# Performance work log

Measured on AMD Instinct MI355X. Metric: run time of the kernel, lower is better.

## Reference

```python
import jax, jax.numpy as jnp
import numpy as np

DIM = 768; NH = 8; G = 14; N = G * G + 1; B = 64; PD = DIM // 16; HID = 4 * DIM
SCOPES = (1, 4, 7)


def _build_adj(fs, scope):
    # windowed adjacency on an fs x fs grid, padded with an always-on ACM (class) token
    idx = np.arange(fs)
    ii, jj = np.meshgrid(idx, idx, indexing='ij')
    ri, rj = ii.ravel(), jj.ravel()
    a = ((np.abs(ri[:, None] - ri[None, :]) <= scope) & (np.abs(rj[:, None] - rj[None, :]) <= scope)).astype(np.float32)
    out = np.ones((fs * fs + 1, fs * fs + 1), np.float32)
    out[1:, 1:] = a
    return out


def _prior_adj():
    # loop=0 -> loop1=loop2=0, repeat = NH//4; heads get [adj1,adj1,adj2,adj2,adj3,adj3,ones,ones]
    rep = NH // 4
    mats = [_build_adj(G, s) for s in SCOPES] + [np.ones((N, N), np.float32)]
    return np.stack([m for m in mats for _ in range(rep)], 0)


def _rel_idx():
    coords = np.stack(np.meshgrid(np.arange(G), np.arange(G), indexing='ij')).reshape(2, -1)
    rel = (coords[:, :, None] - coords[:, None, :]).transpose(1, 2, 0).copy()
    rel[..., 0] += G - 1
    rel[..., 1] += G - 1
    rel[..., 0] *= 2 * G - 1
    idx = rel.sum(-1)
    out = np.full((N, N), (2 * G - 1) ** 2 + 1, np.int32)
    out[1:, 1:] = idx
    return out


def _biases():
    r = np.arange(-G, G + 1)  # arange(1-(G+1), G+1)
    g = np.stack(np.meshgrid(r, r, indexing='ij')).reshape(2, -1).T
    return g.astype(np.float32)  # ((2G+1)^2, 2)


def setup_inputs():
    key = jax.random.key(0)
    ks = iter(jax.random.split(key, 32))
    rn = lambda *s: jax.random.normal(next(ks), s, jnp.float32) * 0.02
    return dict(
        x=jax.random.normal(next(ks), (B, N, DIM), jnp.float32),
        norm1_w=jnp.ones(DIM), norm1_b=jnp.zeros(DIM),
        qkv_w=rn(3 * DIM, DIM),
        scale=10.0 * jnp.ones((NH, 1, 1)),
        pp_w=rn(PD, 2), pp_b=jnp.zeros(PD),
        ln1_w=jnp.ones(PD), ln1_b=jnp.zeros(PD), fcp1_w=rn(PD, PD), fcp1_b=jnp.zeros(PD),
        ln2_w=jnp.ones(PD), ln2_b=jnp.zeros(PD), fcp2_w=rn(PD, PD), fcp2_b=jnp.zeros(PD),
        ln3_w=jnp.ones(PD), ln3_b=jnp.zeros(PD), fcp3_w=rn(NH, PD), fcp3_b=jnp.zeros(NH),
        pre_w=rn(NH, NH) + jnp.eye(NH), post_w=rn(NH, NH) + jnp.eye(NH),
        proj_w=rn(DIM, DIM), proj_b=jnp.zeros(DIM),
        norm2_w=jnp.ones(DIM), norm2_b=jnp.zeros(DIM),
        m1_w=rn(HID, DIM), m1_b=jnp.zeros(HID),
        m2_w=rn(DIM, HID), m2_b=jnp.zeros(DIM),
        prior_adj=jnp.asarray(_prior_adj()),
        biases=jnp.asarray(_biases()),
        rel_idx=jnp.asarray(_rel_idx()),
    )


def _ln(x, w, b, eps=1e-5):
    m = x.mean(-1, keepdims=True)
    v = ((x - m) ** 2).mean(-1, keepdims=True)
    return (x - m) / jnp.sqrt(v + eps) * w + b


def _l2n(x, eps=1e-12):
    return x / jnp.maximum(jnp.linalg.norm(x, axis=-1, keepdims=True), eps)


def reference(x, norm1_w, norm1_b, qkv_w, scale, pp_w, pp_b, ln1_w, ln1_b, fcp1_w, fcp1_b, ln2_w, ln2_b, fcp2_w, fcp2_b, ln3_w, ln3_b, fcp3_w, fcp3_b, pre_w, post_w, proj_w, proj_b, norm2_w, norm2_b, m1_w, m1_b, m2_w, m2_b, prior_adj, biases, rel_idx):
    Bq, Nq, C = x.shape
    d = C // NH
    h = _ln(x, norm1_w, norm1_b)
    qkv = (h @ qkv_w.T).reshape(Bq, Nq, 3, NH, d).transpose(2, 0, 3, 1, 4)
    q, k, v = qkv[0], qkv[1], qkv[2]  # each (B, NH, N, d)
    attn = jnp.einsum('bhnd,bhmd->bhnm', _l2n(q), _l2n(k)) * jnp.minimum(scale, 100.0)[None]
    p = biases @ pp_w.T + pp_b
    p = jax.nn.relu(_ln(p, ln1_w, ln1_b)) @ fcp1_w.T + fcp1_b
    p = jax.nn.relu(_ln(p, ln2_w, ln2_b)) @ fcp2_w.T + fcp2_b
    p = jax.nn.relu(_ln(p, ln3_w, ln3_b)) @ fcp3_w.T + fcp3_b  # (841, NH)
    rpb = p[rel_idx]  # (N, N, NH)
    attn = attn + rpb.transpose(2, 0, 1)[None]
    attn = jnp.einsum('oh,bhnm->bonm', pre_w, attn)  # 1x1 conv over heads (pre-softmax)
    attn = jnp.where(prior_adj[None] > 0, attn, -1e9)
    attn = jax.nn.softmax(attn, axis=-1)
    attn = jnp.einsum('oh,bhnm->bonm', post_w, attn)  # 1x1 conv over heads (post-softmax)
    out = jnp.einsum('bhnm,bhmd->bhnd', attn, v).transpose(0, 2, 1, 3).reshape(Bq, Nq, C)
    x = x + (out @ proj_w.T + proj_b)
    h2 = _ln(x, norm2_w, norm2_b)
    h2 = jax.nn.gelu(h2 @ m1_w.T + m1_b, approximate=False) @ m2_w.T + m2_b
    return x + h2
```

## Files before the change

kernel.cpp:

```cpp
#include <hip/hip_runtime.h>
#include <hip/hip_bf16.h>
#include <math.h>

typedef __hip_bfloat16 bf16;
typedef __attribute__((ext_vector_type(8))) short bf16x8;
typedef __attribute__((ext_vector_type(4))) float f32x4;

__device__ __forceinline__ float b2f(bf16 x){ return __bfloat162float(x); }
__device__ __forceinline__ bf16  f2b(float x){ return __float2bfloat16(x); }
__device__ __forceinline__ float us2f(unsigned short u){ bf16 t; *(unsigned short*)&t = u; return __bfloat162float(t); }

__device__ __forceinline__ void gld16(const bf16* g, bf16* l){
    __builtin_amdgcn_global_load_lds(
        (const __attribute__((address_space(1))) unsigned int*)g,
        (__attribute__((address_space(3))) unsigned int*)l, 16, 0, 0);
}

#define NTOK 197
#define NBATCH 64
#define NHEAD 8
#define DHEAD 96
#define DIMC 768
#define NROWS (NBATCH * NTOK)
#define VTS 224
#define SMS 200
#define SBS 224
#define MHALF 6304

#define OFF_P   0ull
#define OFF_W   32768ull
#define SZ_QKVW 3538944ull
#define SZ_PRJW 1179648ull
#define SZ_M1W  4718592ull
#define SZ_M2W  4718592ull
#define OFF_H   14188544ull
#define SZ_H    19365888ull
#define OFF_Q   33554432ull
#define OFF_K   52920320ull
#define OFF_V   72286208ull

__global__ __launch_bounds__(256) void w_cvt_all(
    const float* __restrict__ s0, const float* __restrict__ s1,
    const float* __restrict__ s2, const float* __restrict__ s3, bf16* __restrict__ d)
{
    int i = blockIdx.x*256 + threadIdx.x;
    const float* s; int off;
    if (i < 442368){ s=s0; off=i; }
    else if (i < 589824){ s=s1; off=i-442368; }
    else if (i < 1179648){ s=s2; off=i-589824; }
    else { s=s3; off=i-1179648; }
    float4 v = ((const float4*)s)[off];
    bf16 t[4] = {f2b(v.x), f2b(v.y), f2b(v.z), f2b(v.w)};
    ((ushort4*)d)[i] = *(ushort4*)t;
}

__global__ __launch_bounds__(64) void pos_mlp(
    const float* __restrict__ biases, const float* __restrict__ pp_w, const float* __restrict__ pp_b,
    const float* __restrict__ ln1w, const float* __restrict__ ln1b,
    const float* __restrict__ f1w,  const float* __restrict__ f1b,
    const float* __restrict__ ln2w, const float* __restrict__ ln2b,
    const float* __restrict__ f2w,  const float* __restrict__ f2b,
    const float* __restrict__ ln3w, const float* __restrict__ ln3b,
    const float* __restrict__ f3w,  const float* __restrict__ f3b,
    const float* __restrict__ pre_w,
    float* __restrict__ pout)
{
    const int row = blockIdx.x, j = threadIdx.x;
    __shared__ float va[48], vb[48], pf[8];
    float b0 = biases[row*2], b1 = biases[row*2+1];
    if (j < 48) va[j] = b0*pp_w[j*2] + b1*pp_w[j*2+1] + pp_b[j];
    __syncthreads();
    {   float s=0.f, s2=0.f;
        for (int i=0;i<48;i++){ float t=va[i]; s+=t; s2+=t*t; }
        float mean=s*(1.f/48.f), var=s2*(1.f/48.f)-mean*mean, inv=rsqrtf(var+1e-5f);
        float r=0.f;
        if (j < 48){
            r = f1b[j];
            for (int i=0;i<48;i++){
                float t = fmaxf((va[i]-mean)*inv*ln1w[i] + ln1b[i], 0.f);
                r += t * f1w[j*48+i];
            }
        }
        __syncthreads();
        if (j < 48) vb[j] = r;
    }
    __syncthreads();
    {   float s=0.f, s2=0.f;
        for (int i=0;i<48;i++){ float t=vb[i]; s+=t; s2+=t*t; }
        float mean=s*(1.f/48.f), var=s2*(1.f/48.f)-mean*mean, inv=rsqrtf(var+1e-5f);
        float r=0.f;
        if (j < 48){
            r = f2b[j];
            for (int i=0;i<48;i++){
                float t = fmaxf((vb[i]-mean)*inv*ln2w[i] + ln2b[i], 0.f);
                r += t * f2w[j*48+i];
            }
        }
        __syncthreads();
        if (j < 48) va[j] = r;
    }
    __syncthreads();
    {   float s=0.f, s2=0.f;
        for (int i=0;i<48;i++){ float t=va[i]; s+=t; s2+=t*t; }
        float mean=s*(1.f/48.f), var=s2*(1.f/48.f)-mean*mean, inv=rsqrtf(var+1e-5f);
        if (j < 8){
            float r = f3b[j];
            for (int i=0;i<48;i++){
                float t = fmaxf((va[i]-mean)*inv*ln3w[i] + ln3b[i], 0.f);
                r += t * f3w[j*48+i];
            }
            pf[j] = r;
        }
    }
    __syncthreads();
    if (j < 8){
        float s = 0.f;
        #pragma unroll
        for (int hh=0; hh<8; hh++) s += pre_w[j*8+hh]*pf[hh];
        pout[row*8+j] = s;
    }
}

template<typename TIN>
__global__ __launch_bounds__(256) void ln768(
    const TIN* __restrict__ x, const float* __restrict__ w, const float* __restrict__ b,
    bf16* __restrict__ out)
{
    const int row = blockIdx.x, tid = threadIdx.x;
    const int wv = tid >> 6, ln = tid & 63;
    __shared__ float rs[4], rs2[4];
    const TIN* xr = x + (size_t)row * DIMC;
    float v[4] = {0.f,0.f,0.f,0.f};
    if (tid < 192){
        if constexpr (sizeof(TIN) == 4){
            float4 t4 = ((const float4*)xr)[tid];
            v[0]=t4.x; v[1]=t4.y; v[2]=t4.z; v[3]=t4.w;
        } else {
            ushort4 t4 = ((const ushort4*)xr)[tid];
            v[0]=us2f(t4.x); v[1]=us2f(t4.y); v[2]=us2f(t4.z); v[3]=us2f(t4.w);
        }
    }
    float s = v[0]+v[1]+v[2]+v[3];
    float s2 = v[0]*v[0]+v[1]*v[1]+v[2]*v[2]+v[3]*v[3];
    #pragma unroll
    for (int off=32; off; off>>=1){ s += __shfl_xor(s,off,64); s2 += __shfl_xor(s2,off,64); }
    if (ln == 0){ rs[wv]=s; rs2[wv]=s2; }
    __syncthreads();
    s = rs[0]+rs[1]+rs[2]+rs[3]; s2 = rs2[0]+rs2[1]+rs2[2]+rs2[3];
    float mean = s*(1.f/768.f), var = s2*(1.f/768.f) - mean*mean;
    float inv = rsqrtf(var + 1e-5f);
    if (tid < 192){
        float4 w4 = ((const float4*)w)[tid];
        float4 b4 = ((const float4*)b)[tid];
        bf16 o[4];
        o[0] = f2b((v[0]-mean)*inv*w4.x + b4.x);
        o[1] = f2b((v[1]-mean)*inv*w4.y + b4.y);
        o[2] = f2b((v[2]-mean)*inv*w4.z + b4.z);
        o[3] = f2b((v[3]-mean)*inv*w4.w + b4.w);
        ((ushort4*)(out + (size_t)row*DIMC))[tid] = *(ushort4*)o;
    }
}

__global__ __launch_bounds__(256) void l2norm_qk(bf16* __restrict__ q, bf16* __restrict__ k,
                                                 const float* __restrict__ scale)
{
    const int wv = threadIdx.x >> 6, ln = threadIdx.x & 63;
    const int g = ln >> 4, j = ln & 15;
    const size_t NR = (size_t)NBATCH*NHEAD*NTOK;
    size_t row = (size_t)blockIdx.x*16 + wv*4 + g;
    bool isq = row < NR;
    bf16* ptr = isq ? (q + row*DHEAD) : (k + (row-NR)*DHEAD);
    float xv[8];
    float ss = 0.f;
    if (j < 12){
        bf16x8 vv = *(const bf16x8*)(ptr + j*8);
        #pragma unroll
        for (int e=0;e<8;e++){ float f = us2f((unsigned short)vv[e]); xv[e]=f; ss += f*f; }
    }
    #pragma unroll
    for (int off=8; off; off>>=1) ss += __shfl_xor(ss, off, 64);
    float inv = 1.f / fmaxf(sqrtf(ss), 1e-12f);
    if (isq){
        int h = (int)((row / NTOK) & (NHEAD-1));
        inv *= fminf(scale[h], 100.f);
    }
    if (j < 12){
        bf16x8 ov;
        #pragma unroll
        for (int e=0;e<8;e++){ bf16 t = f2b(xv[e]*inv); ov[e] = *(short*)&t; }
        *(bf16x8*)(ptr + j*8) = ov;
    }
}

__global__ __launch_bounds__(256) void attn_mfma(
    const bf16* __restrict__ q, const bf16* __restrict__ k, const bf16* __restrict__ vt,
    const float* __restrict__ p,
    const float* __restrict__ pre_w, const float* __restrict__ post_w,
    bf16* __restrict__ ao)
{
    const int id = blockIdx.x;
    const int r8 = id & 7, t8 = id >> 3;
    const int bx = t8 % 25, b = r8 + 8*(t8/25);
    const int n0 = bx*8;
    const int tid = threadIdx.x, wv = tid>>6, ln = tid&63;
    const int fr = ln&15, fq = ln>>4;
    __shared__ float S[NHEAD*8*SMS];
    __shared__ float s_pre[64], s_post[64];
    bf16* Sb = (bf16*)S;
    if (tid < 64){ s_pre[tid]=pre_w[tid]; s_post[tid]=post_w[tid]; }

    #pragma unroll
    for (int hh=0; hh<2; hh++){
        const int h = wv + hh*4;
        int qr = n0 + fr; if (qr > 196) qr = 196;
        const bf16* qrow = q + ((size_t)(b*NHEAD+h)*NTOK + qr)*DHEAD + fq*8;
        bf16x8 a0 = *(const bf16x8*)(qrow);
        bf16x8 a1 = *(const bf16x8*)(qrow+32);
        bf16x8 a2 = *(const bf16x8*)(qrow+64);
        const bf16* kb0 = k + (size_t)(b*NHEAD+h)*NTOK*DHEAD + fq*8;
        auto krow = [&](int mt){ int nr = mt*16+fr; if (nr>196) nr=196; return kb0 + (size_t)nr*DHEAD; };
        const bf16* kp0 = krow(0);
        bf16x8 c00 = *(const bf16x8*)(kp0), c01 = *(const bf16x8*)(kp0+32), c02 = *(const bf16x8*)(kp0+64);
        const bf16* kp1 = krow(1);
        bf16x8 c10 = *(const bf16x8*)(kp1), c11 = *(const bf16x8*)(kp1+32), c12 = *(const bf16x8*)(kp1+64);
        #pragma unroll
        for (int mt=0; mt<13; mt++){
            bf16x8 p0, p1, p2;
            if (mt < 11){
                const bf16* kn = krow(mt+2);
                p0 = *(const bf16x8*)(kn); p1 = *(const bf16x8*)(kn+32); p2 = *(const bf16x8*)(kn+64);
            }
            f32x4 acc = {};
            acc = __builtin_amdgcn_mfma_f32_16x16x32_bf16(a0, c00, acc,0,0,0);
            acc = __builtin_amdgcn_mfma_f32_16x16x32_bf16(a1, c01, acc,0,0,0);
            acc = __builtin_amdgcn_mfma_f32_16x16x32_bf16(a2, c02, acc,0,0,0);
            int col = mt*16 + fr;
            if (fq < 2 && col < SMS){
                #pragma unroll
                for (int i=0;i<4;i++)
                    S[(h*8 + fq*4+i)*SMS + col] = acc[i];
            }
            c00=c10; c01=c11; c02=c12;
            if (mt < 11){ c10=p0; c11=p1; c12=p2; }
        }
    }
    __syncthreads();

    {
        const int sco[8] = {1,1,4,4,7,7,1000,1000};
        const int nq = tid >> 5, l32 = tid & 31;
        int n = n0 + nq; if (n > 196) n = 196;
        const bool nAlways = (n == 0);
        int ri=0, ci=0;
        if (!nAlways){ ri=(n-1)/14; ci=(n-1)-ri*14; }
        for (int m = l32; m < SMS; m += 32){
            if (m >= 197){
                #pragma unroll
                for (int o=0;o<8;o++) S[(o*8+nq)*SMS+m] = -1e9f;
                continue;
            }
            bool always = nAlways || (m==0);
            int rj=0, cj=0;
            if (m > 0){ rj=(m-1)/14; cj=(m-1)-rj*14; }
            int dr = ri-rj; if (dr<0) dr=-dr;
            int dc = ci-cj; if (dc<0) dc=-dc;
            int idx = always ? 730 : (ri-rj+13)*27 + (ci-cj+13);
            const float* pv = p + idx*8;
            float sh[8];
            #pragma unroll
            for (int h2=0;h2<8;h2++) sh[h2] = S[(h2*8+nq)*SMS+m];
            float ov[8];
            #pragma unroll
            for (int o=0;o<8;o++){
                float v = pv[o];
                #pragma unroll
                for (int h2=0;h2<8;h2++) v += s_pre[o*8+h2]*sh[h2];
                bool on = always || (dr<=sco[o] && dc<=sco[o]);
                ov[o] = on ? v : -1e9f;
            }
            #pragma unroll
            for (int o=0;o<8;o++) S[(o*8+nq)*SMS+m] = ov[o];
        }
    }
    __syncthreads();

    {
        const int g = ln >> 4, l16 = ln & 15;
        #pragma unroll
        for (int rr=0; rr<4; rr++){
            float* row = &S[(wv*16 + rr*4 + g)*SMS];
            float mx = -3e38f;
            for (int m=l16; m<SMS; m+=16) mx = fmaxf(mx, row[m]);
            #pragma unroll
            for (int off=8; off; off>>=1) mx = fmaxf(mx, __shfl_xor(mx,off,64));
            float sum = 0.f;
            for (int m=l16; m<SMS; m+=16){ float e=__expf(row[m]-mx); row[m]=e; sum+=e; }
            #pragma unroll
            for (int off=8; off; off>>=1) sum += __shfl_xor(sum,off,64);
            float inv = 1.f/sum;
            for (int m=l16; m<SMS; m+=16) row[m] *= inv;
        }
    }
    __syncthreads();

    {
        const int nq = tid >> 5, l32 = tid & 31;
        float ov[7][8];
        #pragma unroll
        for (int kk=0; kk<7; kk++){
            int m = l32 + 32*kk;
            if (m < 197){
                float ph[8];
                #pragma unroll
                for (int o=0;o<8;o++) ph[o] = S[(o*8+nq)*SMS+m];
                #pragma unroll
                for (int o2=0;o2<8;o2++){
                    float v=0.f;
                    #pragma unroll
                    for (int o=0;o<8;o++) v += s_post[o2*8+o]*ph[o];
                    ov[kk][o2]=v;
                }
            }
        }
        __syncthreads();
        #pragma unroll
        for (int kk=0; kk<7; kk++){
            int m = l32 + 32*kk;
            #pragma unroll
            for (int o=0;o<8;o++)
                Sb[(o*8+nq)*SBS + m] = (m < 197) ? f2b(ov[kk][o]) : f2b(0.f);
        }
    }
    __syncthreads();

    const int frA = fr & 7;
    #pragma unroll
    for (int hh=0; hh<2; hh++){
        const int h = wv + hh*4;
        const bf16* vbase = vt + (size_t)(b*NHEAD+h)*DHEAD*VTS;
        bf16x8 pa[7];
        #pragma unroll
        for (int ks=0; ks<7; ks++)
            pa[ks] = *(const bf16x8*)(Sb + (h*8+frA)*SBS + ks*32 + fq*8);
        bf16x8 bv[7], bn[7];
        #pragma unroll
        for (int ks=0; ks<7; ks++)
            bv[ks] = *(const bf16x8*)(vbase + (size_t)fr*VTS + ks*32 + fq*8);
        #pragma unroll
        for (int dt=0; dt<6; dt++){
            if (dt < 5){
                #pragma unroll
                for (int ks=0; ks<7; ks++)
                    bn[ks] = *(const bf16x8*)(vbase + (size_t)((dt+1)*16+fr)*VTS + ks*32 + fq*8);
            }
            f32x4 acc = {};
            #pragma unroll
            for (int ks=0; ks<7; ks++)
                acc = __builtin_amdgcn_mfma_f32_16x16x32_bf16(pa[ks], bv[ks], acc,0,0,0);
            #pragma unroll
            for (int i=0;i<4;i++){
                int nq = fq*4+i, n = n0+nq;
                if (nq < 8 && n < NTOK)
                    ao[((size_t)b*NTOK+n)*DIMC + h*DHEAD + dt*16+fr] = f2b(acc[i]);
            }
            #pragma unroll
            for (int ks=0; ks<7; ks++) bv[ks] = bn[ks];
        }
    }
}

enum { EPI_QKV=0, EPI_X1=1, EPI_GELU=2, EPI_OUT=3 };

template<int EPI>
__global__ __launch_bounds__(256) void gemm128(
    const bf16* __restrict__ A, int lda, int M,
    const bf16* __restrict__ B, int ldb,
    int K,
    const float* __restrict__ bias,
    const float* __restrict__ resid_f,
    const bf16* __restrict__ resid_b,
    float* __restrict__ dst_f,
    bf16* __restrict__ dst_b, int lddb,
    int row_off,
    bf16* __restrict__ qo, bf16* __restrict__ ko, bf16* __restrict__ vto)
{
    __shared__ bf16 As[2*128*32];
    __shared__ bf16 Bs[2*128*32];
    const int tid = threadIdx.x;
    const int wv = tid >> 6, ln = tid & 63;
    const int fr = ln & 15, fq = ln >> 4;
    const int wr = (wv & 1)*64, wc = (wv >> 1)*64;
    const int m0 = blockIdx.y*128, n0 = blockIdx.x*128;
    const int lnrow = ln >> 2, lncol = (ln & 3)*8;
    f32x4 acc[4][4] = {};
    for (int k0=0; k0<K; k0+=64){
        #pragma unroll
        for (int t=0;t<2;t++){
            #pragma unroll
            for (int c=0;c<2;c++){
                int rA = m0 + (c*4+wv)*16 + lnrow;
                if (rA >= M) rA = M-1;
                gld16(A + (size_t)rA*lda + k0 + t*32 + lncol, &As[t*4096 + (c*4+wv)*16*32]);
                int rB = n0 + (c*4+wv)*16 + lnrow;
                gld16(B + (size_t)rB*ldb + k0 + t*32 + lncol, &Bs[t*4096 + (c*4+wv)*16*32]);
            }
        }
        __syncthreads();
        #pragma unroll
        for (int t=0;t<2;t++){
            bf16x8 af[4], bfv[4];
            #pragma unroll
            for (int i=0;i<4;i++){
                af[i]  = *(const bf16x8*)&As[t*4096 + (wr + i*16 + fr)*32 + fq*8];
                bfv[i] = *(const bf16x8*)&Bs[t*4096 + (wc + i*16 + fr)*32 + fq*8];
            }
            #pragma unroll
            for (int mi=0;mi<4;mi++)
                #pragma unroll
                for (int ni=0;ni<4;ni++)
                    acc[mi][ni] = __builtin_amdgcn_mfma_f32_16x16x32_bf16(af[mi], bfv[ni], acc[mi][ni],0,0,0);
        }
        __syncthreads();
    }
    #pragma unroll
    for (int mi=0;mi<4;mi++){
        #pragma unroll
        for (int ni=0;ni<4;ni++){
            #pragma unroll
            for (int i=0;i<4;i++){
                int row = m0 + wr + mi*16 + fq*4 + i;
                int col = n0 + wc + ni*16 + fr;
                if (row >= M) continue;
                float val = acc[mi][ni][i];
                if constexpr (EPI == EPI_QKV){
                    int which = col/768, rem = col - which*768;
                    int hh = rem/96, di = rem - hh*96;
                    int bb = row/NTOK, nn = row - bb*NTOK;
                    if (which == 0)      qo[(((size_t)bb*NHEAD+hh)*NTOK+nn)*DHEAD + di] = f2b(val);
                    else if (which == 1) ko[(((size_t)bb*NHEAD+hh)*NTOK+nn)*DHEAD + di] = f2b(val);
                    else {
                        vto[(((size_t)bb*NHEAD+hh)*DHEAD+di)*VTS + nn] = f2b(val);
                        if (nn < VTS - NTOK)
                            vto[(((size_t)bb*NHEAD+hh)*DHEAD+di)*VTS + NTOK + nn] = f2b(0.f);
                    }
                } else if constexpr (EPI == EPI_X1){
                    dst_b[(size_t)row*DIMC + col] = f2b(val + bias[col] + resid_f[(size_t)row*DIMC + col]);
                } else if constexpr (EPI == EPI_GELU){
                    float t = val + bias[col];
                    t = 0.5f*t*(1.f + erff(t*0.70710678118654752f));
                    dst_b[(size_t)row*lddb + col] = f2b(t);
                } else {
                    size_t g = (size_t)(row + row_off)*DIMC + col;
                    dst_f[g] = val + bias[col] + b2f(resid_b[g]);
                }
            }
        }
    }
}

extern "C" void kernel_launch(void* const* d_in, const int* in_sizes, int n_in,
                              void* d_out, int out_size, void* d_ws, size_t ws_size,
                              hipStream_t stream)
{
    const float* x        = (const float*)d_in[0];
    const float* norm1_w  = (const float*)d_in[1];
    const float* norm1_b  = (const float*)d_in[2];
    const float* qkv_w    = (const float*)d_in[3];
    const float* scale    = (const float*)d_in[4];
    const float* pp_w     = (const float*)d_in[5];
    const float* pp_b     = (const float*)d_in[6];
    const float* ln1_w    = (const float*)d_in[7];
    const float* ln1_b    = (const float*)d_in[8];
    const float* fcp1_w   = (const float*)d_in[9];
    const float* fcp1_b   = (const float*)d_in[10];
    const float* ln2_w    = (const float*)d_in[11];
    const float* ln2_b    = (const float*)d_in[12];
    const float* fcp2_w   = (const float*)d_in[13];
    const float* fcp2_b   = (const float*)d_in[14];
    const float* ln3_w    = (const float*)d_in[15];
    const float* ln3_b    = (const float*)d_in[16];
    const float* fcp3_w   = (const float*)d_in[17];
    const float* fcp3_b   = (const float*)d_in[18];
    const float* pre_w    = (const float*)d_in[19];
    const float* post_w   = (const float*)d_in[20];
    const float* proj_w   = (const float*)d_in[21];
    const float* proj_b   = (const float*)d_in[22];
    const float* nrm2_w   = (const float*)d_in[23];
    const float* nrm2_b   = (const float*)d_in[24];
    const float* m1_w     = (const float*)d_in[25];
    const float* m1_b     = (const float*)d_in[26];
    const float* m2_w     = (const float*)d_in[27];
    const float* m2_b     = (const float*)d_in[28];
    const float* biases   = (const float*)d_in[30];
    float* out = (float*)d_out;

    char* ws = (char*)d_ws;
    float* p      = (float*)(ws + OFF_P);
    bf16*  qkvw_b = (bf16*)(ws + OFF_W);
    bf16*  prjw_b = (bf16*)(ws + OFF_W + SZ_QKVW);
    bf16*  m1w_b  = (bf16*)(ws + OFF_W + SZ_QKVW + SZ_PRJW);
    bf16*  m2w_b  = (bf16*)(ws + OFF_W + SZ_QKVW + SZ_PRJW + SZ_M1W);
    bf16*  h   = (bf16*)(ws + OFF_H);
    bf16*  qb  = (bf16*)(ws + OFF_Q);
    bf16*  kb  = (bf16*)(ws + OFF_K);
    bf16*  vt  = (bf16*)(ws + OFF_V);
    bf16*  ao  = (bf16*)(ws + OFF_H);
    bf16*  x1b = (bf16*)(ws + OFF_V);
    bf16*  h2  = (bf16*)(ws + OFF_K);
    bf16*  mid = (bf16*)(ws + OFF_H);

    w_cvt_all<<<6912, 256, 0, stream>>>(qkv_w, proj_w, m1_w, m2_w, qkvw_b);
    pos_mlp<<<841, 64, 0, stream>>>(biases, pp_w, pp_b, ln1_w, ln1_b, fcp1_w, fcp1_b,
                                    ln2_w, ln2_b, fcp2_w, fcp2_b, ln3_w, ln3_b, fcp3_w, fcp3_b,
                                    pre_w, p);
    ln768<float><<<NROWS, 256, 0, stream>>>(x, norm1_w, norm1_b, h);
    gemm128<EPI_QKV><<<dim3(18, 99), 256, 0, stream>>>(
        h, DIMC, NROWS, qkvw_b, DIMC, DIMC, nullptr, nullptr, nullptr, nullptr,
        nullptr, 0, 0, qb, kb, vt);
    l2norm_qk<<<(NBATCH*NHEAD*NTOK*2)/16, 256, 0, stream>>>(qb, kb, scale);
    attn_mfma<<<1600, 256, 0, stream>>>(qb, kb, vt, p, pre_w, post_w, ao);
    gemm128<EPI_X1><<<dim3(6, 99), 256, 0, stream>>>(
        ao, DIMC, NROWS, prjw_b, DIMC, DIMC, proj_b, x, nullptr, nullptr,
        x1b, 0, 0, nullptr, nullptr, nullptr);
    ln768<bf16><<<NROWS, 256, 0, stream>>>(x1b, nrm2_w, nrm2_b, h2);
    for (int c=0; c<2; c++){
        const int r0 = c*MHALF;
        gemm128<EPI_GELU><<<dim3(24, 50), 256, 0, stream>>>(
            h2 + (size_t)r0*DIMC, DIMC, MHALF, m1w_b, DIMC, DIMC, m1_b,
            nullptr, nullptr, nullptr, mid, 3072, 0, nullptr, nullptr, nullptr);
        gemm128<EPI_OUT><<<dim3(6, 50), 256, 0, stream>>>(
            mid, 3072, MHALF, m2w_b, 3072, 3072, m2_b,
            nullptr, x1b, out, nullptr, 0, r0, nullptr, nullptr, nullptr);
    }
    (void)in_sizes; (void)n_in; (void)out_size; (void)ws_size;
}
```

Baseline: 787.1 us.

## Keep attention logits in registers for softmax and remap GEMM blocks per XCD

```diff
diff --git a/kernel.cpp b/kernel.cpp
--- a/kernel.cpp
+++ b/kernel.cpp
@@ -246,17 +246,23 @@
     }
     __syncthreads();
 
+    const int nq = tid >> 5, l32 = tid & 31;
+    float p_[7][8];
+    float ml[8];
+    #pragma unroll
+    for (int o=0;o<8;o++) ml[o] = -3.0e38f;
     {
         const int sco[8] = {1,1,4,4,7,7,1000,1000};
-        const int nq = tid >> 5, l32 = tid & 31;
         int n = n0 + nq; if (n > 196) n = 196;
         const bool nAlways = (n == 0);
         int ri=0, ci=0;
         if (!nAlways){ ri=(n-1)/14; ci=(n-1)-ri*14; }
-        for (int m = l32; m < SMS; m += 32){
+        #pragma unroll
+        for (int kk=0; kk<7; kk++){
+            int m = l32 + 32*kk;
             if (m >= 197){
                 #pragma unroll
-                for (int o=0;o<8;o++) S[(o*8+nq)*SMS+m] = -1e9f;
+                for (int o=0;o<8;o++) p_[kk][o] = -1e9f;
                 continue;
             }
             bool always = nAlways || (m==0);
@@ -269,66 +275,60 @@
             float sh[8];
             #pragma unroll
             for (int h2=0;h2<8;h2++) sh[h2] = S[(h2*8+nq)*SMS+m];
-            float ov[8];
             #pragma unroll
             for (int o=0;o<8;o++){
                 float v = pv[o];
                 #pragma unroll
                 for (int h2=0;h2<8;h2++) v += s_pre[o*8+h2]*sh[h2];
                 bool on = always || (dr<=sco[o] && dc<=sco[o]);
-                ov[o] = on ? v : -1e9f;
-            }
-            #pragma unroll
-            for (int o=0;o<8;o++) S[(o*8+nq)*SMS+m] = ov[o];
-        }
-    }
-    __syncthreads();
-
+                v = on ? v : -1e9f;
+                p_[kk][o] = v;
+                ml[o] = fmaxf(ml[o], v);
+            }
+        }
+    }
+    __syncthreads();
+
+    float invl[8];
     {
-        const int g = ln >> 4, l16 = ln & 15;
-        #pragma unroll
-        for (int rr=0; rr<4; rr++){
-            float* row = &S[(wv*16 + rr*4 + g)*SMS];
-            float mx = -3e38f;
-            for (int m=l16; m<SMS; m+=16) mx = fmaxf(mx, row[m]);
-            #pragma unroll
-            for (int off=8; off; off>>=1) mx = fmaxf(mx, __shfl_xor(mx,off,64));
-            float sum = 0.f;
-            for (int m=l16; m<SMS; m+=16){ float e=__expf(row[m]-mx); row[m]=e; sum+=e; }
-            #pragma unroll
-            for (int off=8; off; off>>=1) sum += __shfl_xor(sum,off,64);
-            float inv = 1.f/sum;
-            for (int m=l16; m<SMS; m+=16) row[m] *= inv;
-        }
-    }
-    __syncthreads();
-
-    {
-        const int nq = tid >> 5, l32 = tid & 31;
-        float ov[7][8];
-        #pragma unroll
-        for (int kk=0; kk<7; kk++){
-            int m = l32 + 32*kk;
-            if (m < 197){
-                float ph[8];
-                #pragma unroll
-                for (int o=0;o<8;o++) ph[o] = S[(o*8+nq)*SMS+m];
-                #pragma unroll
-                for (int o2=0;o2<8;o2++){
-                    float v=0.f;
-                    #pragma unroll
-                    for (int o=0;o<8;o++) v += s_post[o2*8+o]*ph[o];
-                    ov[kk][o2]=v;
-                }
-            }
-        }
-        __syncthreads();
-        #pragma unroll
-        for (int kk=0; kk<7; kk++){
-            int m = l32 + 32*kk;
-            #pragma unroll
-            for (int o=0;o<8;o++)
-                Sb[(o*8+nq)*SBS + m] = (m < 197) ? f2b(ov[kk][o]) : f2b(0.f);
+        #pragma unroll
+        for (int o=0;o<8;o++){
+            float mx = ml[o];
+            #pragma unroll
+            for (int off=16; off; off>>=1) mx = fmaxf(mx, __shfl_xor(mx, off, 64));
+            ml[o] = mx;
+        }
+        float sm[8];
+        #pragma unroll
+        for (int o=0;o<8;o++) sm[o]=0.f;
+        #pragma unroll
+        for (int kk=0;kk<7;kk++){
+            #pragma unroll
+            for (int o=0;o<8;o++){
+                float e = __expf(p_[kk][o] - ml[o]);
+                p_[kk][o] = e; sm[o] += e;
+            }
+        }
+        #pragma unroll
+        for (int o=0;o<8;o++){
+            float s = sm[o];
+            #pragma unroll
+            for (int off=16; off; off>>=1) s += __shfl_xor(s, off, 64);
+            invl[o] = 1.f/s;
+        }
+    }
+    #pragma unroll
+    for (int kk=0;kk<7;kk++){
+        int m = l32 + 32*kk;
+        float qn[8];
+        #pragma unroll
+        for (int o=0;o<8;o++) qn[o] = p_[kk][o]*invl[o];
+        #pragma unroll
+        for (int o2=0;o2<8;o2++){
+            float v=0.f;
+            #pragma unroll
+            for (int o=0;o<8;o++) v += s_post[o2*8+o]*qn[o];
+            Sb[(o2*8+nq)*SBS + m] = f2b(v);
         }
     }
     __syncthreads();
@@ -359,8 +359,8 @@
                 acc = __builtin_amdgcn_mfma_f32_16x16x32_bf16(pa[ks], bv[ks], acc,0,0,0);
             #pragma unroll
             for (int i=0;i<4;i++){
-                int nq = fq*4+i, n = n0+nq;
-                if (nq < 8 && n < NTOK)
+                int nqq = fq*4+i, n = n0+nqq;
+                if (nqq < 8 && n < NTOK)
                     ao[((size_t)b*NTOK+n)*DIMC + h*DHEAD + dt*16+fr] = f2b(acc[i]);
             }
             #pragma unroll
@@ -382,7 +382,8 @@
     float* __restrict__ dst_f,
     bf16* __restrict__ dst_b, int lddb,
     int row_off,
-    bf16* __restrict__ qo, bf16* __restrict__ ko, bf16* __restrict__ vto)
+    bf16* __restrict__ qo, bf16* __restrict__ ko, bf16* __restrict__ vto,
+    int nbx)
 {
     __shared__ bf16 As[2*128*32];
     __shared__ bf16 Bs[2*128*32];
@@ -390,7 +391,12 @@
     const int wv = tid >> 6, ln = tid & 63;
     const int fr = ln & 15, fq = ln >> 4;
     const int wr = (wv & 1)*64, wc = (wv >> 1)*64;
-    const int m0 = blockIdx.y*128, n0 = blockIdx.x*128;
+    const int nwgs = (int)gridDim.x;
+    const int xcd = blockIdx.x & 7;
+    const int qq = nwgs >> 3, rr = nwgs & 7;
+    const int wg = (xcd < rr ? xcd*(qq+1) : rr*(qq+1) + (xcd-rr)*qq) + ((int)blockIdx.x >> 3);
+    const int byi = wg / nbx, bxi = wg - byi*nbx;
+    const int m0 = byi*128, n0 = bxi*128;
     const int lnrow = ln >> 2, lncol = (ln & 3)*8;
     f32x4 acc[4][4] = {};
     for (int k0=0; k0<K; k0+=64){
@@ -514,23 +520,23 @@
                                     ln2_w, ln2_b, fcp2_w, fcp2_b, ln3_w, ln3_b, fcp3_w, fcp3_b,
                                     pre_w, p);
     ln768<float><<<NROWS, 256, 0, stream>>>(x, norm1_w, norm1_b, h);
-    gemm128<EPI_QKV><<<dim3(18, 99), 256, 0, stream>>>(
+    gemm128<EPI_QKV><<<18*99, 256, 0, stream>>>(
         h, DIMC, NROWS, qkvw_b, DIMC, DIMC, nullptr, nullptr, nullptr, nullptr,
-        nullptr, 0, 0, qb, kb, vt);
+        nullptr, 0, 0, qb, kb, vt, 18);
     l2norm_qk<<<(NBATCH*NHEAD*NTOK*2)/16, 256, 0, stream>>>(qb, kb, scale);
     attn_mfma<<<1600, 256, 0, stream>>>(qb, kb, vt, p, pre_w, post_w, ao);
-    gemm128<EPI_X1><<<dim3(6, 99), 256, 0, stream>>>(
+    gemm128<EPI_X1><<<6*99, 256, 0, stream>>>(
         ao, DIMC, NROWS, prjw_b, DIMC, DIMC, proj_b, x, nullptr, nullptr,
-        x1b, 0, 0, nullptr, nullptr, nullptr);
+        x1b, 0, 0, nullptr, nullptr, nullptr, 6);
     ln768<bf16><<<NROWS, 256, 0, stream>>>(x1b, nrm2_w, nrm2_b, h2);
     for (int c=0; c<2; c++){
         const int r0 = c*MHALF;
-        gemm128<EPI_GELU><<<dim3(24, 50), 256, 0, stream>>>(
+        gemm128<EPI_GELU><<<24*50, 256, 0, stream>>>(
             h2 + (size_t)r0*DIMC, DIMC, MHALF, m1w_b, DIMC, DIMC, m1_b,
-            nullptr, nullptr, nullptr, mid, 3072, 0, nullptr, nullptr, nullptr);
-        gemm128<EPI_OUT><<<dim3(6, 50), 256, 0, stream>>>(
+            nullptr, nullptr, nullptr, mid, 3072, 0, nullptr, nullptr, nullptr, 24);
+        gemm128<EPI_OUT><<<6*50, 256, 0, stream>>>(
             mid, 3072, MHALF, m2w_b, 3072, 3072, m2_b,
-            nullptr, x1b, out, nullptr, 0, r0, nullptr, nullptr, nullptr);
+            nullptr, x1b, out, nullptr, 0, r0, nullptr, nullptr, nullptr, 6);
     }
     (void)in_sizes; (void)n_in; (void)out_size; (void)ws_size;
 }
```

After: 786.6 us. Within noise of the previous version (-0.1%).
